# Kernel tuning notes

Hardware: AMD Instinct MI355X
Metric: run time of the kernel (lower is better)

Reference implementation:

```python
import jax, jax.numpy as jnp
import numpy as np

DIM = 1024
HEADS = 16
HEAD_DIM = DIM // HEADS
DFF = 4 * DIM
EPS = 1e-6


def _layernorm(x, scale, bias):
    mu = jnp.mean(x, axis=-1, keepdims=True)
    var = jnp.mean(jnp.square(x - mu), axis=-1, keepdims=True)
    return (x - mu) * jax.lax.rsqrt(var + EPS) * scale + bias


def setup_inputs() -> dict:
    key = jax.random.key(0)
    ks = jax.random.split(key, 8)
    d = {}
    d["x"] = jax.random.normal(ks[0], (4, 2048, DIM), dtype=jnp.float32)
    # LayerNorm params
    d["ln1_scale"] = jnp.ones((DIM,), jnp.float32)
    d["ln1_bias"] = jnp.zeros((DIM,), jnp.float32)
    d["ln2_scale"] = jnp.ones((DIM,), jnp.float32)
    d["ln2_bias"] = jnp.zeros((DIM,), jnp.float32)
    # Attention params
    d["qkv_w"] = jax.random.normal(ks[1], (DIM, 3 * DIM), jnp.float32) * (DIM ** -0.5)
    d["qkv_b"] = jnp.zeros((3 * DIM,), jnp.float32)
    d["proj_w"] = jax.random.normal(ks[2], (DIM, DIM), jnp.float32) * (DIM ** -0.5)
    d["proj_b"] = jnp.zeros((DIM,), jnp.float32)
    # MLP params
    d["fc1_w"] = jax.random.normal(ks[3], (DIM, DFF), jnp.float32) * (DIM ** -0.5)
    d["fc1_b"] = jnp.zeros((DFF,), jnp.float32)
    d["fc2_w"] = jax.random.normal(ks[4], (DFF, DIM), jnp.float32) * (DFF ** -0.5)
    d["fc2_b"] = jnp.zeros((DIM,), jnp.float32)
    return d


def reference(x, ln1_scale, ln1_bias, ln2_scale, ln2_bias,
              qkv_w, qkv_b, proj_w, proj_b,
              fc1_w, fc1_b, fc2_w, fc2_b):
    B, S, D = x.shape
    scale = HEAD_DIM ** -0.5

    # --- Attention sub-block (pre-LN) ---
    h = _layernorm(x, ln1_scale, ln1_bias)
    qkv = h @ qkv_w + qkv_b                                  # [B,S,3D]
    qkv = qkv.reshape(B, S, 3, HEADS, HEAD_DIM)
    qkv = qkv.transpose(2, 0, 3, 1, 4)                       # [3,B,H,S,hd]
    q, k, v = qkv[0], qkv[1], qkv[2]
    attn = jnp.einsum('bhqd,bhkd->bhqk', q, k) * scale       # [B,H,S,S]
    attn = jax.nn.softmax(attn, axis=-1)
    out = jnp.einsum('bhqk,bhkd->bhqd', attn, v)             # [B,H,S,hd]
    out = out.transpose(0, 2, 1, 3).reshape(B, S, D)
    out = out @ proj_w + proj_b
    x = x + out

    # --- MLP sub-block (pre-LN) ---
    h = _layernorm(x, ln2_scale, ln2_bias)
    h = jax.nn.gelu(h @ fc1_w + fc1_b)
    h = h @ fc2_w + fc2_b
    return x + h
```

## Files before the change

### kernel.cpp

```cpp
#include <hip/hip_runtime.h>
#include <hip/hip_bf16.h>

typedef __attribute__((ext_vector_type(4))) float f32x4;
typedef __attribute__((ext_vector_type(16))) float f32x16;
typedef __attribute__((ext_vector_type(8))) short bf16x8;

__device__ __forceinline__ unsigned short f2bf(float f) {
    return __bfloat16_as_ushort(__float2bfloat16(f));
}

typedef __attribute__((address_space(1))) const unsigned char* gas_ptr;
typedef __attribute__((address_space(3))) unsigned char* las_ptr;
__device__ __forceinline__ void gload16(const void* g, void* l) {
    __builtin_amdgcn_global_load_lds((gas_ptr)g, (las_ptr)l, 16, 0, 0);
}

__device__ __forceinline__ unsigned cvt_pk_bf16(float lo, float hi) {
    unsigned r;
    asm("v_cvt_pk_bf16_f32 %0, %1, %2" : "=v"(r) : "v"(lo), "v"(hi));
    return r;
}

__global__ __launch_bounds__(256) void ln_kernel(
    const float* __restrict__ x, const float* __restrict__ scale,
    const float* __restrict__ bias, unsigned short* __restrict__ out)
{
    int row = blockIdx.x;
    const float* xr = x + (size_t)row * 1024;
    int t = threadIdx.x;
    float4 v = ((const float4*)xr)[t];
    float s  = v.x + v.y + v.z + v.w;
    float ss = v.x*v.x + v.y*v.y + v.z*v.z + v.w*v.w;
    #pragma unroll
    for (int m = 32; m; m >>= 1) { s += __shfl_down(s, m); ss += __shfl_down(ss, m); }
    __shared__ float red[8];
    int wid = t >> 6;
    if ((t & 63) == 0) { red[wid*2] = s; red[wid*2+1] = ss; }
    __syncthreads();
    s  = red[0] + red[2] + red[4] + red[6];
    ss = red[1] + red[3] + red[5] + red[7];
    float mu  = s * (1.0f/1024.0f);
    float var = ss * (1.0f/1024.0f) - mu*mu;
    float inv = rsqrtf(var + 1e-6f);
    float4 sc = ((const float4*)scale)[t];
    float4 bi = ((const float4*)bias)[t];
    ushort4 o;
    o.x = f2bf((v.x - mu)*inv*sc.x + bi.x);
    o.y = f2bf((v.y - mu)*inv*sc.y + bi.y);
    o.z = f2bf((v.z - mu)*inv*sc.z + bi.z);
    o.w = f2bf((v.w - mu)*inv*sc.w + bi.w);
    ((ushort4*)(out + (size_t)row * 1024))[t] = o;
}

__global__ __launch_bounds__(256) void transpose_kernel(
    const float* __restrict__ W, unsigned short* __restrict__ Wt, int K, int N)
{
    __shared__ float tile[32][33];
    int n0 = blockIdx.x * 32, k0 = blockIdx.y * 32;
    int tx = threadIdx.x, ty = threadIdx.y;
    #pragma unroll
    for (int j = 0; j < 32; j += 8)
        tile[ty + j][tx] = W[(size_t)(k0 + ty + j) * N + n0 + tx];
    __syncthreads();
    #pragma unroll
    for (int j = 0; j < 32; j += 8)
        Wt[(size_t)(n0 + ty + j) * K + k0 + tx] = f2bf(tile[tx][ty + j]);
}

template<int EPI>
__global__ __launch_bounds__(256, 4) void gemm_kernel(
    const unsigned short* __restrict__ A,
    const unsigned short* __restrict__ Bt,
    const float* __restrict__ bias,
    const float* __restrict__ res,
    void* __restrict__ out,
    unsigned short* __restrict__ vtout,
    int M, int N, int K)
{
    __shared__ __align__(16) unsigned short Al[128 * 64];
    __shared__ __align__(16) unsigned short Bl[128 * 64];

    int t = threadIdx.x;
    int wid = t >> 6, lane = t & 63;
    int wr = wid >> 1, wc = wid & 1;
    int l15 = lane & 15, lg = lane >> 4;

    int gx = gridDim.x;
    int nwg = gx * gridDim.y;
    int orig = blockIdx.y * gx + blockIdx.x;
    int cpx = nwg >> 3;
    int wg = (orig & 7) * cpx + (orig >> 3);
    int bx = wg % gx, by = wg / gx;
    int brow = by * 128, bcol = bx * 128;

    f32x4 acc[4][4] = {};

    int sr  = t >> 3;
    int scb = (t & 7) * 16;
    int sce = (scb ^ ((sr & 7) << 4)) >> 1;
    const size_t aoff = (size_t)(brow + sr) * K + sce;
    const size_t boff = (size_t)(bcol + sr) * K + sce;
    char* la = (char*)Al + (wid << 10);
    char* lb = (char*)Bl + (wid << 10);

    int nk = K >> 6;
    int rsw = (l15 & 7) << 4;
    for (int kt = 0; kt < nk; kt++) {
        int k0 = kt << 6;
        __syncthreads();
        #pragma unroll
        for (int i = 0; i < 4; i++) {
            gload16(A  + aoff + (size_t)(i * 32) * K + k0, la + i * 4096);
            gload16(Bt + boff + (size_t)(i * 32) * K + k0, lb + i * 4096);
        }
        __syncthreads();
        #pragma unroll
        for (int kf = 0; kf < 2; kf++) {
            bf16x8 af[4], bfr[4];
            #pragma unroll
            for (int mf = 0; mf < 4; mf++)
                af[mf] = *(const bf16x8*)((const char*)Al + (wr*64 + mf*16 + l15)*128 + ((kf*64 + lg*16) ^ rsw));
            #pragma unroll
            for (int nf = 0; nf < 4; nf++)
                bfr[nf] = *(const bf16x8*)((const char*)Bl + (wc*64 + nf*16 + l15)*128 + ((kf*64 + lg*16) ^ rsw));
            __builtin_amdgcn_s_setprio(1);
            #pragma unroll
            for (int mf = 0; mf < 4; mf++)
                #pragma unroll
                for (int nf = 0; nf < 4; nf++)
                    acc[mf][nf] = __builtin_amdgcn_mfma_f32_16x16x32_bf16(
                        af[mf], bfr[nf], acc[mf][nf], 0, 0, 0);
            __builtin_amdgcn_s_setprio(0);
        }
    }

    #pragma unroll
    for (int mi = 0; mi < 4; mi++) {
        #pragma unroll
        for (int nf = 0; nf < 4; nf++) {
            int col = bcol + wc * 64 + nf * 16 + l15;
            float bs = bias[col];
            #pragma unroll
            for (int r = 0; r < 4; r++) {
                int row = brow + wr * 64 + mi * 16 + lg * 4 + r;
                size_t idx = (size_t)row * N + col;
                float v = acc[mi][nf][r] + bs;
                if (EPI == 1) {
                    ((float*)out)[idx] = v + res[idx];
                } else if (EPI == 2) {
                    float u = v + 0.044715f * v * v * v;
                    float e = __builtin_amdgcn_exp2f(-2.3022077f * u);
                    float g = v * __builtin_amdgcn_rcpf(1.0f + e);
                    ((unsigned short*)out)[idx] = f2bf(g);
                } else {
                    float vq = (col < 1024) ? v * 0.18033688f : v;
                    unsigned short bv = f2bf(vq);
                    ((unsigned short*)out)[idx] = bv;
                    if (col >= 2048) {
                        int hd = col - 2048;
                        int b = row >> 11, s = row & 2047;
                        vtout[((size_t)((b << 4) + (hd >> 6)) * 64 + (hd & 63)) * 2048 + s] = bv;
                    }
                }
            }
        }
    }
}

__global__ __launch_bounds__(512, 2) void attn_kernel(
    const unsigned short* __restrict__ qkv, const unsigned short* __restrict__ vt,
    unsigned short* __restrict__ ctx)
{
    __shared__ unsigned short Kl[2][4096];
    __shared__ unsigned short Vl[2][4096];

    int t = threadIdx.x;
    int wid = t >> 6, lane = t & 63;
    int l31 = lane & 31, half = lane >> 5;

    int n = blockIdx.y * 8 + blockIdx.x;
    int m = n >> 3;
    int qt = m & 7;
    int bh = (n & 7) + ((m >> 3) << 3);
    int b = bh >> 4, h = bh & 15;
    int qr0 = qt * 256 + wid * 32;

    const size_t qbase = (size_t)b * 2048 * 3072 + (size_t)h * 64;
    const unsigned short* vbase = vt + (size_t)bh * 64 * 2048;

    bf16x8 qf[4];
    #pragma unroll
    for (int ds = 0; ds < 4; ds++)
        qf[ds] = *(const bf16x8*)(qkv + qbase + (size_t)(qr0 + l31) * 3072 + ds*16 + half*8);

    f32x16 ot0 = {}, ot1 = {};
    float lrun = 0.0f;

    int srow = t >> 3;
    int ssw = ((t & 7) * 16) ^ ((srow & 7) << 4);
    const unsigned short* kg = qkv + qbase + 1024 + (size_t)srow * 3072 + (ssw >> 1);
    const unsigned short* vg = vbase + (size_t)srow * 2048 + (ssw >> 1);

    gload16(kg, (char*)Kl[0] + t * 16);
    gload16(vg, (char*)Vl[0] + t * 16);
    __syncthreads();

    int cur = 0;
    for (int kt = 0; kt < 32; kt++) {
        if (kt < 31) {
            gload16(kg + (size_t)(kt + 1) * 64 * 3072, (char*)Kl[cur ^ 1] + t * 16);
            gload16(vg + (kt + 1) * 64,               (char*)Vl[cur ^ 1] + t * 16);
        }

        const char* Kb = (const char*)Kl[cur];
        const char* Vb = (const char*)Vl[cur];
        int sw = (l31 & 7) << 4;

        f32x16 st0 = {}, st1 = {};
        __builtin_amdgcn_s_setprio(1);
        #pragma unroll
        for (int ds = 0; ds < 4; ds++) {
            int colb = ds*32 + half*16;
            bf16x8 k0 = *(const bf16x8*)(Kb + l31*128 + (colb ^ sw));
            bf16x8 k1 = *(const bf16x8*)(Kb + (32 + l31)*128 + (colb ^ sw));
            st0 = __builtin_amdgcn_mfma_f32_32x32x16_bf16(k0, qf[ds], st0, 0, 0, 0);
            st1 = __builtin_amdgcn_mfma_f32_32x32x16_bf16(k1, qf[ds], st1, 0, 0, 0);
        }
        __builtin_amdgcn_s_setprio(0);

        unsigned w0[8], w1[8];
        float sum = 0.0f;
        {
            float e[16];
            #pragma unroll
            for (int r = 0; r < 16; r++) { e[r] = __builtin_amdgcn_exp2f(st0[r]); sum += e[r]; }
            #pragma unroll
            for (int p = 0; p < 8; p++) w0[p] = cvt_pk_bf16(e[2*p], e[2*p+1]);
            #pragma unroll
            for (int r = 0; r < 16; r++) { e[r] = __builtin_amdgcn_exp2f(st1[r]); sum += e[r]; }
            #pragma unroll
            for (int p = 0; p < 8; p++) w1[p] = cvt_pk_bf16(e[2*p], e[2*p+1]);
        }
        lrun += sum;

        __builtin_amdgcn_s_setprio(1);
        #pragma unroll
        for (int ks = 0; ks < 4; ks++) {
            union { unsigned u[4]; bf16x8 v; } pf;
            unsigned* w = (ks < 2) ? w0 : w1;
            int o4 = (ks & 1) * 4;
            pf.u[0] = w[o4 + 0]; pf.u[1] = w[o4 + 1]; pf.u[2] = w[o4 + 2]; pf.u[3] = w[o4 + 3];
            int lo = ks*32 + half*8;
            union { unsigned long long d[2]; bf16x8 v; } va, vb;
            va.d[0] = *(const unsigned long long*)(Vb + l31*128 + (lo ^ sw));
            va.d[1] = *(const unsigned long long*)(Vb + l31*128 + ((lo + 16) ^ sw));
            vb.d[0] = *(const unsigned long long*)(Vb + (32 + l31)*128 + (lo ^ sw));
            vb.d[1] = *(const unsigned long long*)(Vb + (32 + l31)*128 + ((lo + 16) ^ sw));
            ot0 = __builtin_amdgcn_mfma_f32_32x32x16_bf16(va.v, pf.v, ot0, 0, 0, 0);
            ot1 = __builtin_amdgcn_mfma_f32_32x32x16_bf16(vb.v, pf.v, ot1, 0, 0, 0);
        }
        __builtin_amdgcn_s_setprio(0);

        __syncthreads();
        cur ^= 1;
    }

    float ltot = lrun + __shfl_xor(lrun, 32);
    float rl = 1.0f / ltot;
    size_t cb = (size_t)b * 2048 * 1024 + (size_t)(qr0 + l31) * 1024 + (size_t)h * 64;
    #pragma unroll
    for (int r = 0; r < 16; r++) {
        int d = (r & 3) + 8 * (r >> 2) + 4 * half;
        ctx[cb + d]      = f2bf(ot0[r] * rl);
        ctx[cb + 32 + d] = f2bf(ot1[r] * rl);
    }
}

extern "C" void kernel_launch(void* const* d_in, const int* in_sizes, int n_in,
                              void* d_out, int out_size, void* d_ws, size_t ws_size,
                              hipStream_t stream) {
    const float* x      = (const float*)d_in[0];
    const float* ln1_s  = (const float*)d_in[1];
    const float* ln1_b  = (const float*)d_in[2];
    const float* ln2_s  = (const float*)d_in[3];
    const float* ln2_b  = (const float*)d_in[4];
    const float* qkv_w  = (const float*)d_in[5];
    const float* qkv_b  = (const float*)d_in[6];
    const float* proj_w = (const float*)d_in[7];
    const float* proj_b = (const float*)d_in[8];
    const float* fc1_w  = (const float*)d_in[9];
    const float* fc1_b  = (const float*)d_in[10];
    const float* fc2_w  = (const float*)d_in[11];
    const float* fc2_b  = (const float*)d_in[12];
    float* out = (float*)d_out;

    char* ws = (char*)d_ws;
    unsigned short* vtb  = (unsigned short*)(ws + 0);
    float*          x1   = (float*)(ws + 0);
    unsigned short* h    = (unsigned short*)(ws + (size_t)32 * 1024 * 1024);
    unsigned short* qkvb = (unsigned short*)(ws + (size_t)48 * 1024 * 1024);
    unsigned short* gbuf = (unsigned short*)(ws + (size_t)48 * 1024 * 1024);
    unsigned short* ctxb = (unsigned short*)(ws + (size_t)96 * 1024 * 1024);
    unsigned short* wT   = (unsigned short*)(ws + (size_t)112 * 1024 * 1024);

    dim3 tb(32, 8);

    transpose_kernel<<<dim3(96, 32), tb, 0, stream>>>(qkv_w, wT, 1024, 3072);
    ln_kernel<<<8192, 256, 0, stream>>>(x, ln1_s, ln1_b, h);
    gemm_kernel<3><<<dim3(24, 64), 256, 0, stream>>>(h, wT, qkv_b, nullptr, qkvb, vtb, 8192, 3072, 1024);
    attn_kernel<<<dim3(8, 64), 512, 0, stream>>>(qkvb, vtb, ctxb);
    transpose_kernel<<<dim3(32, 32), tb, 0, stream>>>(proj_w, wT, 1024, 1024);
    gemm_kernel<1><<<dim3(8, 64), 256, 0, stream>>>(ctxb, wT, proj_b, x, x1, nullptr, 8192, 1024, 1024);
    ln_kernel<<<8192, 256, 0, stream>>>(x1, ln2_s, ln2_b, h);
    transpose_kernel<<<dim3(128, 32), tb, 0, stream>>>(fc1_w, wT, 1024, 4096);
    gemm_kernel<2><<<dim3(32, 64), 256, 0, stream>>>(h, wT, fc1_b, nullptr, gbuf, nullptr, 8192, 4096, 1024);
    transpose_kernel<<<dim3(32, 128), tb, 0, stream>>>(fc2_w, wT, 4096, 1024);
    gemm_kernel<1><<<dim3(8, 64), 256, 0, stream>>>(gbuf, wT, fc2_b, x1, out, nullptr, 8192, 1024, 4096);
}
```

Measured before the change: 382.2 us.

## Add 256x256 eight-wave double-buffered GEMM for QKV and FC1 projections

Adds a new GEMM kernel with 256x256 output tiles, 512 threads (8 waves) and double-buffered LDS. It interleaves global-to-LDS prefetch of the next K-tile with four MFMA phases per iteration, using vmcnt waits and barriers. The kernel is used for the wide QKV and FC1 GEMMs, with the epilogue factored into a shared helper. The larger tiles raise arithmetic intensity and overlap loads with compute. In exchange they use 128KB of LDS per block and launch fewer workgroups (384 and 512), which risks tail imbalance across the CUs.

```diff
diff --git a/kernel.cpp b/kernel.cpp
--- a/kernel.cpp
+++ b/kernel.cpp
@@ -68,6 +68,160 @@
 }
 
 template<int EPI>
+__device__ __forceinline__ void epi_store(
+    float v, int row, int col, int N,
+    const float* __restrict__ res, void* __restrict__ out,
+    unsigned short* __restrict__ vtout)
+{
+    size_t idx = (size_t)row * N + col;
+    if (EPI == 1) {
+        ((float*)out)[idx] = v + res[idx];
+    } else if (EPI == 2) {
+        float u = v + 0.044715f * v * v * v;
+        float e = __builtin_amdgcn_exp2f(-2.3022077f * u);
+        float g = v * __builtin_amdgcn_rcpf(1.0f + e);
+        ((unsigned short*)out)[idx] = f2bf(g);
+    } else {
+        float vq = (col < 1024) ? v * 0.18033688f : v;
+        unsigned short bv = f2bf(vq);
+        ((unsigned short*)out)[idx] = bv;
+        if (col >= 2048) {
+            int hd = col - 2048;
+            int b = row >> 11, s = row & 2047;
+            vtout[((size_t)((b << 4) + (hd >> 6)) * 64 + (hd & 63)) * 2048 + s] = bv;
+        }
+    }
+}
+
+template<int EPI>
+__global__ __launch_bounds__(512, 2) void gemm8p_kernel(
+    const unsigned short* __restrict__ A,
+    const unsigned short* __restrict__ Bt,
+    const float* __restrict__ bias,
+    const float* __restrict__ res,
+    void* __restrict__ out,
+    unsigned short* __restrict__ vtout,
+    int M, int N, int K)
+{
+    __shared__ __align__(16) unsigned short Al[2][256 * 64];
+    __shared__ __align__(16) unsigned short Bl[2][256 * 64];
+
+    int t = threadIdx.x;
+    int wid = t >> 6, lane = t & 63;
+    int wr = wid >> 2, wc = wid & 3;
+    int l15 = lane & 15, lg = lane >> 4;
+
+    int gx = gridDim.x;
+    int nwg = gx * gridDim.y;
+    int orig = blockIdx.y * gx + blockIdx.x;
+    int cpx = nwg >> 3;
+    int wg = (orig & 7) * cpx + (orig >> 3);
+    int bx = wg % gx, by = wg / gx;
+    int brow = by * 256, bcol = bx * 256;
+
+    f32x4 acc[2][4][2][2] = {};
+
+    int sr  = t >> 3;
+    int scb = (t & 7) * 16;
+    int sce = (scb ^ ((sr & 7) << 4)) >> 1;
+    const size_t aoff = (size_t)(brow + sr) * K + sce;
+    const size_t boff = (size_t)(bcol + sr) * K + sce;
+    int wb = wid << 10;
+
+    auto stgA = [&](int d, int kt2, int q) {
+        gload16(A + aoff + (size_t)(q * 64) * K + (kt2 << 6),
+                (char*)Al[d] + q * 8192 + wb);
+    };
+    auto stgB = [&](int d, int kt2, int q) {
+        gload16(Bt + boff + (size_t)(q * 64) * K + (kt2 << 6),
+                (char*)Bl[d] + q * 8192 + wb);
+    };
+
+    int nk = K >> 6;
+    stgB(0,0,0); stgB(0,0,1); stgB(0,0,2); stgB(0,0,3);
+    stgA(0,0,0); stgA(0,0,2);
+    stgA(0,0,1); stgA(0,0,3);
+    asm volatile("s_waitcnt vmcnt(2)" ::: "memory");
+    __builtin_amdgcn_s_barrier();
+
+    int rsw = (l15 & 7) << 4;
+    for (int kt = 0; kt < nk; kt++) {
+        int d = kt & 1, nd = d ^ 1;
+        bool st = (kt + 1 < nk);
+        const char* Ab = (const char*)Al[d];
+        const char* Bb = (const char*)Bl[d];
+        bf16x8 af[4][2], bf[2][2];
+
+        #pragma unroll
+        for (int mq = 0; mq < 2; mq++) {
+            #pragma unroll
+            for (int nh = 0; nh < 2; nh++) {
+                if (nh == 0) {
+                    #pragma unroll
+                    for (int mf = 0; mf < 4; mf++) {
+                        int ra = wr*128 + mq*64 + mf*16 + l15;
+                        #pragma unroll
+                        for (int kk = 0; kk < 2; kk++)
+                            af[mf][kk] = *(const bf16x8*)(Ab + ra*128 + ((kk*64 + lg*16) ^ rsw));
+                    }
+                }
+                #pragma unroll
+                for (int nf = 0; nf < 2; nf++) {
+                    int rb = wc*64 + nh*32 + nf*16 + l15;
+                    #pragma unroll
+                    for (int kk = 0; kk < 2; kk++)
+                        bf[nf][kk] = *(const bf16x8*)(Bb + rb*128 + ((kk*64 + lg*16) ^ rsw));
+                }
+                if (st) {
+                    int p = mq*2 + nh;
+                    if (p == 0)      { stgB(nd, kt+1, 0); stgB(nd, kt+1, 1); }
+                    else if (p == 1) { stgB(nd, kt+1, 2); stgB(nd, kt+1, 3); }
+                    else if (p == 2) { stgA(nd, kt+1, 0); stgA(nd, kt+1, 2); }
+                    else             { stgA(nd, kt+1, 1); stgA(nd, kt+1, 3); }
+                }
+                __builtin_amdgcn_s_barrier();
+                asm volatile("s_waitcnt lgkmcnt(0)" ::: "memory");
+                __builtin_amdgcn_sched_barrier(0);
+                __builtin_amdgcn_s_setprio(1);
+                #pragma unroll
+                for (int mf = 0; mf < 4; mf++)
+                    #pragma unroll
+                    for (int nf = 0; nf < 2; nf++)
+                        #pragma unroll
+                        for (int kk = 0; kk < 2; kk++)
+                            acc[mq][mf][nh][nf] = __builtin_amdgcn_mfma_f32_16x16x32_bf16(
+                                af[mf][kk], bf[nf][kk], acc[mq][mf][nh][nf], 0, 0, 0);
+                __builtin_amdgcn_s_setprio(0);
+                if (mq == 0 && nh == 1) {
+                    if (st) asm volatile("s_waitcnt vmcnt(4)" ::: "memory");
+                    else    asm volatile("s_waitcnt vmcnt(0)" ::: "memory");
+                } else if (mq == 1 && nh == 1 && st) {
+                    asm volatile("s_waitcnt vmcnt(2)" ::: "memory");
+                }
+                __builtin_amdgcn_s_barrier();
+            }
+        }
+    }
+
+    #pragma unroll
+    for (int mq = 0; mq < 2; mq++)
+        #pragma unroll
+        for (int mf = 0; mf < 4; mf++)
+            #pragma unroll
+            for (int nh = 0; nh < 2; nh++)
+                #pragma unroll
+                for (int nf = 0; nf < 2; nf++) {
+                    int col = bcol + wc*64 + nh*32 + nf*16 + l15;
+                    float bs = bias[col];
+                    #pragma unroll
+                    for (int r = 0; r < 4; r++) {
+                        int row = brow + wr*128 + mq*64 + mf*16 + lg*4 + r;
+                        epi_store<EPI>(acc[mq][mf][nh][nf][r] + bs, row, col, N, res, out, vtout);
+                    }
+                }
+}
+
+template<int EPI>
 __global__ __launch_bounds__(256, 4) void gemm_kernel(
     const unsigned short* __restrict__ A,
     const unsigned short* __restrict__ Bt,
@@ -143,25 +297,7 @@
             #pragma unroll
             for (int r = 0; r < 4; r++) {
                 int row = brow + wr * 64 + mi * 16 + lg * 4 + r;
-                size_t idx = (size_t)row * N + col;
-                float v = acc[mi][nf][r] + bs;
-                if (EPI == 1) {
-                    ((float*)out)[idx] = v + res[idx];
-                } else if (EPI == 2) {
-                    float u = v + 0.044715f * v * v * v;
-                    float e = __builtin_amdgcn_exp2f(-2.3022077f * u);
-                    float g = v * __builtin_amdgcn_rcpf(1.0f + e);
-                    ((unsigned short*)out)[idx] = f2bf(g);
-                } else {
-                    float vq = (col < 1024) ? v * 0.18033688f : v;
-                    unsigned short bv = f2bf(vq);
-                    ((unsigned short*)out)[idx] = bv;
-                    if (col >= 2048) {
-                        int hd = col - 2048;
-                        int b = row >> 11, s = row & 2047;
-                        vtout[((size_t)((b << 4) + (hd >> 6)) * 64 + (hd & 63)) * 2048 + s] = bv;
-                    }
-                }
+                epi_store<EPI>(acc[mi][nf][r] + bs, row, col, N, res, out, vtout);
             }
         }
     }
@@ -307,13 +443,13 @@
 
     transpose_kernel<<<dim3(96, 32), tb, 0, stream>>>(qkv_w, wT, 1024, 3072);
     ln_kernel<<<8192, 256, 0, stream>>>(x, ln1_s, ln1_b, h);
-    gemm_kernel<3><<<dim3(24, 64), 256, 0, stream>>>(h, wT, qkv_b, nullptr, qkvb, vtb, 8192, 3072, 1024);
+    gemm8p_kernel<3><<<dim3(12, 32), 512, 0, stream>>>(h, wT, qkv_b, nullptr, qkvb, vtb, 8192, 3072, 1024);
     attn_kernel<<<dim3(8, 64), 512, 0, stream>>>(qkvb, vtb, ctxb);
     transpose_kernel<<<dim3(32, 32), tb, 0, stream>>>(proj_w, wT, 1024, 1024);
     gemm_kernel<1><<<dim3(8, 64), 256, 0, stream>>>(ctxb, wT, proj_b, x, x1, nullptr, 8192, 1024, 1024);
     ln_kernel<<<8192, 256, 0, stream>>>(x1, ln2_s, ln2_b, h);
     transpose_kernel<<<dim3(128, 32), tb, 0, stream>>>(fc1_w, wT, 1024, 4096);
-    gemm_kernel<2><<<dim3(32, 64), 256, 0, stream>>>(h, wT, fc1_b, nullptr, gbuf, nullptr, 8192, 4096, 1024);
+    gemm8p_kernel<2><<<dim3(16, 32), 512, 0, stream>>>(h, wT, fc1_b, nullptr, gbuf, nullptr, 8192, 4096, 1024);
     transpose_kernel<<<dim3(32, 128), tb, 0, stream>>>(fc2_w, wT, 4096, 1024);
     gemm_kernel<1><<<dim3(8, 64), 256, 0, stream>>>(gbuf, wT, fc2_b, x1, out, nullptr, 8192, 1024, 4096);
 }
```

New measurement: 387.2 us. About the same (+1.3%).
